# Kernel tuning notes

Measured on AMD Instinct MI355X. Metric: run time of the kernel, lower is better.

The kernel has to match this reference:

```python
import jax, jax.numpy as jnp
import numpy as np

BIN_SIZE = 16
B, C, H, W = 32, 256, 64, 64


def _make_grid(lab):
    # Faithful vectorization of the per-batch loop in the torch module.
    # index = arange(bin) - bin//2
    idx = jnp.arange(BIN_SIZE, dtype=lab.dtype) - (BIN_SIZE // 2)
    # mesh_y[b, j] = 2*idx[j]*lab[b,0,3]/bin + (lab[b,0,1]*2 - 1)
    mesh_y = 2.0 * idx[None, :] * lab[:, 0, 3, None] / BIN_SIZE + (lab[:, 0, 1, None] * 2.0 - 1.0)
    # mesh_x[b, i] = 2*idx[i]*lab[b,0,4]/bin + (lab[b,0,2]*2 - 1)
    mesh_x = 2.0 * idx[None, :] * lab[:, 0, 4, None] / BIN_SIZE + (lab[:, 0, 2, None] * 2.0 - 1.0)
    b = lab.shape[0]
    # torch: grid_x, grid_y = meshgrid(mesh_x, mesh_y) with 'ij' indexing;
    # mesh_box[b,i,j,0] = grid_y[i,j] = mesh_y[j]; mesh_box[b,i,j,1] = grid_x[i,j] = mesh_x[i]
    g0 = jnp.broadcast_to(mesh_y[:, None, :], (b, BIN_SIZE, BIN_SIZE))  # x-coord channel
    g1 = jnp.broadcast_to(mesh_x[:, :, None], (b, BIN_SIZE, BIN_SIZE))  # y-coord channel
    return jnp.stack([g0, g1], axis=-1)  # [B, bin, bin, 2]


def _grid_sample(feat, grid):
    # Bilinear grid_sample, padding_mode='zeros', align_corners=False (torch defaults).
    Bb, Cc, Hh, Ww = feat.shape
    x = ((grid[..., 0] + 1.0) * Ww - 1.0) * 0.5  # [B, Hg, Wg]
    y = ((grid[..., 1] + 1.0) * Hh - 1.0) * 0.5
    x0f = jnp.floor(x)
    y0f = jnp.floor(y)
    x0 = x0f.astype(jnp.int32)
    y0 = y0f.astype(jnp.int32)
    x1 = x0 + 1
    y1 = y0 + 1
    wx1 = x - x0f
    wx0 = 1.0 - wx1
    wy1 = y - y0f
    wy0 = 1.0 - wy1
    bidx = jnp.arange(Bb)[:, None, None]

    def corner(xi, yi, wgt):
        valid = ((xi >= 0) & (xi < Ww) & (yi >= 0) & (yi < Hh)).astype(feat.dtype)
        xc = jnp.clip(xi, 0, Ww - 1)
        yc = jnp.clip(yi, 0, Hh - 1)
        v = feat[bidx, :, yc, xc]  # [B, Hg, Wg, C] (advanced indices pulled front)
        return v * (wgt * valid)[..., None]

    out = (corner(x0, y0, wx0 * wy0) + corner(x1, y0, wx1 * wy0)
           + corner(x0, y1, wx0 * wy1) + corner(x1, y1, wx1 * wy1))
    return jnp.transpose(out, (0, 3, 1, 2))  # [B, C, Hg, Wg]


def setup_inputs() -> dict:
    key = jax.random.key(0)
    k1, k2, k3 = jax.random.split(key, 3)
    original_features = jax.random.normal(k1, (B, C, H, W), dtype=jnp.float32)
    attack_features = jax.random.uniform(k2, (B, C, H, W), dtype=jnp.float32)
    lab = jax.random.uniform(k3, (B, 1, 5), dtype=jnp.float32)  # normalized box coords
    return {"original_features": original_features, "lab": lab, "attack_features": attack_features}


def reference(original_features, lab, attack_features):
    grid = _make_grid(lab)
    output_1 = _grid_sample(original_features, grid)
    output_2 = _grid_sample(attack_features, grid)
    return (output_1, output_2)
```

## Files before the change

### kernel.cpp

```cpp
#include <hip/hip_runtime.h>

#define Bsz 32
#define Csz 256
#define Hsz 64
#define Wsz 64
#define BIN 16

__global__ __launch_bounds__(256) void roi_feature_kernel(
    const float* __restrict__ orig,
    const float* __restrict__ lab,
    const float* __restrict__ attk,
    float* __restrict__ out)
{
    const int tid = blockIdx.x * blockDim.x + threadIdx.x;
    const int j = tid & (BIN - 1);
    const int i = (tid >> 4) & (BIN - 1);
    const int c = (tid >> 8) & (Csz - 1);
    const int b = tid >> 16;

    const float* lb = lab + b * 5;
    const float l1 = lb[1], l2 = lb[2], l3 = lb[3], l4 = lb[4];

    const float gx = 2.0f * (float)(j - BIN / 2) * l3 / (float)BIN + (l1 * 2.0f - 1.0f);
    const float gy = 2.0f * (float)(i - BIN / 2) * l4 / (float)BIN + (l2 * 2.0f - 1.0f);

    const float x = ((gx + 1.0f) * (float)Wsz - 1.0f) * 0.5f;
    const float y = ((gy + 1.0f) * (float)Hsz - 1.0f) * 0.5f;

    const float x0f = floorf(x);
    const float y0f = floorf(y);
    const int x0 = (int)x0f;
    const int y0 = (int)y0f;
    const int x1 = x0 + 1;
    const int y1 = y0 + 1;
    const float wx1 = x - x0f, wx0 = 1.0f - wx1;
    const float wy1 = y - y0f, wy0 = 1.0f - wy1;

    const size_t plane = (size_t)(b * Csz + c) * (Hsz * Wsz);
    const float* __restrict__ f0 = orig + plane;
    const float* __restrict__ f1 = attk + plane;

    float acc0 = 0.0f, acc1 = 0.0f;
#pragma unroll
    for (int k = 0; k < 4; ++k) {
        const int xi = (k & 1) ? x1 : x0;
        const int yi = (k & 2) ? y1 : y0;
        const float w = ((k & 1) ? wx1 : wx0) * ((k & 2) ? wy1 : wy0);
        const bool valid = (xi >= 0) && (xi < Wsz) && (yi >= 0) && (yi < Hsz);
        const int xc = min(max(xi, 0), Wsz - 1);
        const int yc = min(max(yi, 0), Hsz - 1);
        const float wv = valid ? w : 0.0f;
        const int off = yc * Wsz + xc;
        acc0 += f0[off] * wv;
        acc1 += f1[off] * wv;
    }

    out[tid] = acc0;
    out[tid + (size_t)Bsz * Csz * BIN * BIN] = acc1;
}

extern "C" void kernel_launch(void* const* d_in, const int* in_sizes, int n_in,
                              void* d_out, int out_size, void* d_ws, size_t ws_size,
                              hipStream_t stream) {
    const float* orig = (const float*)d_in[0];
    const float* lab  = (const float*)d_in[1];
    const float* attk = (const float*)d_in[2];
    float* out = (float*)d_out;

    const int total = Bsz * Csz * BIN * BIN;
    roi_feature_kernel<<<total / 256, 256, 0, stream>>>(orig, lab, attk, out);
}
```

Baseline: 237.2 us.

## Stage needed feature rows of each plane into LDS with float4 loads before sampling

```diff
diff --git a/kernel.cpp b/kernel.cpp
--- a/kernel.cpp
+++ b/kernel.cpp
@@ -5,6 +5,7 @@
 #define Hsz 64
 #define Wsz 64
 #define BIN 16
+#define ROWSTRIDE 68
 
 __global__ __launch_bounds__(256) void roi_feature_kernel(
     const float* __restrict__ orig,
@@ -12,20 +13,46 @@
     const float* __restrict__ attk,
     float* __restrict__ out)
 {
-    const int tid = blockIdx.x * blockDim.x + threadIdx.x;
-    const int j = tid & (BIN - 1);
-    const int i = (tid >> 4) & (BIN - 1);
-    const int c = (tid >> 8) & (Csz - 1);
-    const int b = tid >> 16;
+    __shared__ float lds[2][Hsz][ROWSTRIDE];
+
+    const int tid = threadIdx.x;
+    const int bc  = blockIdx.x;
+    const int b   = bc >> 8;
 
     const float* lb = lab + b * 5;
     const float l1 = lb[1], l2 = lb[2], l3 = lb[3], l4 = lb[4];
 
-    const float gx = 2.0f * (float)(j - BIN / 2) * l3 / (float)BIN + (l1 * 2.0f - 1.0f);
-    const float gy = 2.0f * (float)(i - BIN / 2) * l4 / (float)BIN + (l2 * 2.0f - 1.0f);
+    const float ya = 4.0f * l4;
+    const float yb = 64.0f * l2 - 0.5f;
+    const float y_lo = fminf(ya * (0 - 8) + yb, ya * (15 - 8) + yb);
+    const float y_hi = fmaxf(ya * (0 - 8) + yb, ya * (15 - 8) + yb);
 
-    const float x = ((gx + 1.0f) * (float)Wsz - 1.0f) * 0.5f;
-    const float y = ((gy + 1.0f) * (float)Hsz - 1.0f) * 0.5f;
+    int ry0 = (int)floorf(y_lo);
+    int ry1 = (int)floorf(y_hi) + 1;
+    ry0 = min(max(ry0, 0), Hsz - 1);
+    ry1 = min(max(ry1, ry0), Hsz - 1);
+    const int nrows = ry1 - ry0 + 1;
+
+    const size_t plane = (size_t)bc * (Hsz * Wsz);
+    const float* __restrict__ f0 = orig + plane + ry0 * Wsz;
+    const float* __restrict__ f1 = attk + plane + ry0 * Wsz;
+
+    const int nvec = nrows * (Wsz / 4);
+    for (int v = tid; v < nvec; v += 256) {
+        const int row = v >> 4;
+        const int col = (v & 15) * 4;
+        const float4 a = *(const float4*)(f0 + row * Wsz + col);
+        const float4 c = *(const float4*)(f1 + row * Wsz + col);
+        *(float4*)&lds[0][row][col] = a;
+        *(float4*)&lds[1][row][col] = c;
+    }
+    __syncthreads();
+
+    const int j = tid & (BIN - 1);
+    const int i = tid >> 4;
+
+    const float x = 4.0f * l3 * (float)(j - 8) + 64.0f * l1 - 0.5f;
+    const float y = ya * (float)(i - 8) + yb;
 
     const float x0f = floorf(x);
     const float y0f = floorf(y);
@@ -36,10 +63,6 @@
     const float wx1 = x - x0f, wx0 = 1.0f - wx1;
     const float wy1 = y - y0f, wy0 = 1.0f - wy1;
 
-    const size_t plane = (size_t)(b * Csz + c) * (Hsz * Wsz);
-    const float* __restrict__ f0 = orig + plane;
-    const float* __restrict__ f1 = attk + plane;
-
     float acc0 = 0.0f, acc1 = 0.0f;
 #pragma unroll
     for (int k = 0; k < 4; ++k) {
@@ -47,16 +70,16 @@
         const int yi = (k & 2) ? y1 : y0;
         const float w = ((k & 1) ? wx1 : wx0) * ((k & 2) ? wy1 : wy0);
         const bool valid = (xi >= 0) && (xi < Wsz) && (yi >= 0) && (yi < Hsz);
+        const float wv = valid ? w : 0.0f;
         const int xc = min(max(xi, 0), Wsz - 1);
-        const int yc = min(max(yi, 0), Hsz - 1);
-        const float wv = valid ? w : 0.0f;
-        const int off = yc * Wsz + xc;
-        acc0 += f0[off] * wv;
-        acc1 += f1[off] * wv;
+        const int yc = min(max(yi, 0), Hsz - 1) - ry0;
+        acc0 += lds[0][yc][xc] * wv;
+        acc1 += lds[1][yc][xc] * wv;
     }
 
-    out[tid] = acc0;
-    out[tid + (size_t)Bsz * Csz * BIN * BIN] = acc1;
+    const int gidx = bc * 256 + tid;
+    out[gidx] = acc0;
+    out[gidx + Bsz * Csz * BIN * BIN] = acc1;
 }
 
 extern "C" void kernel_launch(void* const* d_in, const int* in_sizes, int n_in,
@@ -67,6 +90,5 @@
     const float* attk = (const float*)d_in[2];
     float* out = (float*)d_out;
 
-    const int total = Bsz * Csz * BIN * BIN;
-    roi_feature_kernel<<<total / 256, 256, 0, stream>>>(orig, lab, attk, out);
+    roi_feature_kernel<<<Bsz * Csz, 256, 0, stream>>>(orig, lab, attk, out);
 }
```

Result: no change. 240.9 us (+1.6%).
